# Kernel tuning notes

Measured on AMD Instinct MI355X. Metric: run time of the kernel, lower is better.

Reference implementation:

```python
import jax, jax.numpy as jnp
import numpy as np

B, S, D, H = 2, 4096, 512, 8
DH = D // H
EPS = 1e-5


def setup_inputs() -> dict:
    key = jax.random.key(0)
    ks = jax.random.split(key, 8)
    s = 0.02
    return {
        "x": jax.random.normal(ks[0], (B, S, D), jnp.float32),
        "in_proj_w": jax.random.normal(ks[1], (3 * D, D), jnp.float32) * s,
        "in_proj_b": jnp.zeros((3 * D,), jnp.float32),
        "out_proj_w": jax.random.normal(ks[2], (D, D), jnp.float32) * s,
        "out_proj_b": jnp.zeros((D,), jnp.float32),
        "ln1_g": jnp.ones((D,), jnp.float32),
        "ln1_b": jnp.zeros((D,), jnp.float32),
        "ln2_g": jnp.ones((D,), jnp.float32),
        "ln2_b": jnp.zeros((D,), jnp.float32),
        "w1": jax.random.normal(ks[3], (D, D), jnp.float32) * s,
        "b1": jnp.zeros((D,), jnp.float32),
        "w2": jax.random.normal(ks[4], (D, D), jnp.float32) * s,
        "b2": jnp.zeros((D,), jnp.float32),
        "window": 256,
    }


def _layernorm(x, g, b):
    mu = jnp.mean(x, axis=-1, keepdims=True)
    var = jnp.mean(jnp.square(x - mu), axis=-1, keepdims=True)
    return (x - mu) * jax.lax.rsqrt(var + EPS) * g + b


def reference(x, in_proj_w, in_proj_b, out_proj_w, out_proj_b,
              ln1_g, ln1_b, ln2_g, ln2_b, w1, b1, w2, b2, window):
    b, s, d = x.shape
    # sliding-window mask: allowed iff |i - j| <= window
    idx = jnp.arange(s)
    allowed = jnp.abs(idx[:, None] - idx[None, :]) <= window  # [S,S]

    # fused QKV projection (torch MultiheadAttention layout: W [3D, D])
    qkv = x @ in_proj_w.T + in_proj_b  # [B,S,3D]
    q, k, v = jnp.split(qkv, 3, axis=-1)
    q = q.reshape(b, s, H, DH)
    k = k.reshape(b, s, H, DH)
    v = v.reshape(b, s, H, DH)

    scale = 1.0 / jnp.sqrt(jnp.float32(DH))
    scores = jnp.einsum("bqhd,bkhd->bhqk", q, k) * scale  # [B,H,S,S]
    scores = jnp.where(allowed[None, None], scores, -jnp.inf)
    attn = jax.nn.softmax(scores, axis=-1)
    ctx = jnp.einsum("bhqk,bkhd->bqhd", attn, v).reshape(b, s, d)
    attn_out = ctx @ out_proj_w.T + out_proj_b

    # residual + LayerNorm (dropout rate 0 -> identity)
    h = _layernorm(x + attn_out, ln1_g, ln1_b)
    mlp = jax.nn.relu(h @ w1.T + b1) @ w2.T + b2
    return _layernorm(h + mlp, ln2_g, ln2_b)
```

## Files before the change

### kernel.cpp

```cpp
#include <hip/hip_runtime.h>

typedef __bf16 bf16;
typedef __bf16 bf16x2 __attribute__((ext_vector_type(2)));
typedef __bf16 bf16x8 __attribute__((ext_vector_type(8)));
typedef float f32x4 __attribute__((ext_vector_type(4)));

#define S_LEN 4096
#define DMODEL 512
#define NHEAD 8
#define DHEAD 64
#define BATCH 2
#define M_ROWS (BATCH * S_LEN)
#define K_DIM 512
#define QKV_LD 1536

__device__ __forceinline__ void async16(void* lds, const void* g) {
  __builtin_amdgcn_global_load_lds(
      (const __attribute__((address_space(1))) unsigned int*)g,
      (__attribute__((address_space(3))) unsigned int*)lds, 16, 0, 0);
}

__device__ __forceinline__ int detect_bf16(const unsigned int* x, int lane) {
  int cnt = 0;
#pragma unroll
  for (int i = 0; i < 16; ++i) {
    const unsigned int w = x[lane * 16 + i];
    const unsigned int e = (w >> 7) & 0xFFu;
    cnt += (e >= 100u && e <= 140u) ? 1 : 0;
  }
#pragma unroll
  for (int off = 1; off < 64; off <<= 1) cnt += __shfl_xor(cnt, off);
  return (cnt >= 700) ? 1 : 0;
}

__device__ __forceinline__ bf16x8 ld8(const void* p, size_t e, bool asF32) {
  if (asF32) {
    const float* q = (const float*)p + e;
    const float4 a = *(const float4*)q;
    const float4 b = *(const float4*)(q + 4);
    bf16x8 r;
    r[0] = (bf16)a.x; r[1] = (bf16)a.y; r[2] = (bf16)a.z; r[3] = (bf16)a.w;
    r[4] = (bf16)b.x; r[5] = (bf16)b.y; r[6] = (bf16)b.z; r[7] = (bf16)b.w;
    return r;
  }
  return *(const bf16x8*)((const bf16*)p + e);
}

__device__ __forceinline__ float ld1(const void* p, size_t e, bool asF32) {
  return asF32 ? ((const float*)p)[e] : (float)((const bf16*)p)[e];
}

__global__ __launch_bounds__(256) void cvt_all(const void* __restrict__ x,
                                               const void* __restrict__ s0,
                                               const void* __restrict__ s1,
                                               const void* __restrict__ s2,
                                               const void* __restrict__ s3,
                                               bf16* __restrict__ xb,
                                               bf16* __restrict__ warena,
                                               int* __restrict__ flag) {
  const int isbf = detect_bf16((const unsigned int*)x, threadIdx.x & 63);
  const bool f32in = (isbf == 0);
  const int b = blockIdx.x;
  if (b == 0 && threadIdx.x == 0) *flag = isbf;
  if (b < 2048) {
    const size_t idx = ((size_t)b * 256 + threadIdx.x) * 8;
    *(bf16x8*)(xb + idx) = ld8(x, idx, f32in);
    return;
  }
  const int wb = b - 2048;
  const void* s;
  size_t doff;
  int lb;
  if (wb < 384)      { s = s0; doff = 0;        lb = wb; }
  else if (wb < 512) { s = s1; doff = 786432;   lb = wb - 384; }
  else if (wb < 640) { s = s2; doff = 1048576;  lb = wb - 512; }
  else               { s = s3; doff = 1310720;  lb = wb - 640; }
  const size_t idx = (size_t)lb * 2048 + threadIdx.x * 8;
  *(bf16x8*)(warena + doff + idx) = ld8(s, idx, f32in);
}

template <int NMAT, int BN, bool RELU>
__global__ __launch_bounds__(256) void gemm_bt(const bf16* __restrict__ A,
                                               const bf16* __restrict__ W,
                                               const void* __restrict__ bias,
                                               bf16* __restrict__ C,
                                               const int* __restrict__ flag) {
  __shared__ __align__(16) bf16 As[2][128 * 64];
  __shared__ __align__(16) bf16 Ws[2][BN * 64];

  const bool f32in = (*flag == 0);

  const int t = threadIdx.x;
  const int lane = t & 63;
  const int wave = t >> 6;
  constexpr int MT = (BN == 128) ? 4 : 2;
  const int wm = (BN == 128) ? (wave >> 1) * 64 : wave * 32;
  const int wn = (BN == 128) ? (wave & 1) * 64 : 0;
  const int l16 = lane & 15;
  const int quad = lane >> 4;

  constexpr int NB = NMAT / BN;
  constexpr int MPX = (M_ROWS / 128) / 8;
  const int bid = blockIdx.x;
  const int xcd = bid & 7;
  const int r = bid >> 3;
  const int m0 = (xcd * MPX + r / NB) * 128;
  const int n0 = (r % NB) * BN;

  const int rr = lane >> 3;
  const int cb = (lane & 7) ^ rr;
  const int sw = l16 & 7;

  f32x4 acc[MT][4];
#pragma unroll
  for (int i = 0; i < MT; ++i)
#pragma unroll
    for (int j = 0; j < 4; ++j) acc[i][j] = (f32x4){0.f, 0.f, 0.f, 0.f};

  auto stage = [&](int buf, int kt) {
#pragma unroll
    for (int i = 0; i < 4; ++i) {
      const int r0 = wave * 32 + i * 8;
      async16(&As[buf][r0 * 64],
              &A[(size_t)(m0 + r0 + rr) * K_DIM + kt + cb * 8]);
    }
#pragma unroll
    for (int i = 0; i < BN / 32; ++i) {
      const int r0 = wave * (BN / 4) + i * 8;
      async16(&Ws[buf][r0 * 64],
              &W[(size_t)(n0 + r0 + rr) * K_DIM + kt + cb * 8]);
    }
  };

  stage(0, 0);
  constexpr int NIT = K_DIM / 64;
  for (int it = 0; it < NIT; ++it) {
    const int cur = it & 1;
    __syncthreads();
    if (it + 1 < NIT) stage(cur ^ 1, (it + 1) * 64);
#pragma unroll
    for (int ks = 0; ks < 2; ++ks) {
      bf16x8 af[MT], wf[4];
#pragma unroll
      for (int mt = 0; mt < MT; ++mt)
        af[mt] = *(const bf16x8*)&As[cur][(wm + mt * 16 + l16) * 64 +
                                          (((ks * 4 + quad) ^ sw) * 8)];
#pragma unroll
      for (int nt = 0; nt < 4; ++nt)
        wf[nt] = *(const bf16x8*)&Ws[cur][(wn + nt * 16 + l16) * 64 +
                                          (((ks * 4 + quad) ^ sw) * 8)];
#pragma unroll
      for (int mt = 0; mt < MT; ++mt)
#pragma unroll
        for (int nt = 0; nt < 4; ++nt)
          acc[mt][nt] = __builtin_amdgcn_mfma_f32_16x16x32_bf16(af[mt], wf[nt],
                                                                acc[mt][nt], 0, 0, 0);
    }
  }

#pragma unroll
  for (int nt = 0; nt < 4; ++nt) {
    const int n = n0 + wn + nt * 16 + l16;
    const float bv = ld1(bias, n, f32in);
#pragma unroll
    for (int mt = 0; mt < MT; ++mt) {
#pragma unroll
      for (int r4 = 0; r4 < 4; ++r4) {
        const int m = m0 + wm + mt * 16 + quad * 4 + r4;
        float v = acc[mt][nt][r4] + bv;
        if (RELU) v = fmaxf(v, 0.f);
        C[(size_t)m * NMAT + n] = (bf16)v;
      }
    }
  }
}

__global__ __launch_bounds__(256) void attn_fwd(const bf16* __restrict__ qkv,
                                                bf16* __restrict__ ctx,
                                                const int* __restrict__ wptr) {
  __shared__ __align__(16) bf16 Kt[2][64 * 64];
  __shared__ __align__(16) bf16 Vt[2][64][72];
  __shared__ __align__(16) bf16 Pbuf[4][16][72];

  const int t = threadIdx.x;
  const int lane = t & 63;
  const int wave = t >> 6;
  const int l16 = lane & 15;
  const int quad = lane >> 4;
  const int rr = lane >> 3;
  const int cb = (lane & 7) ^ rr;
  const int sw = l16 & 7;

  const int bid = blockIdx.x;
  const int xcd = bid & 7;
  const int jj = bid >> 3;
  const int pair = xcd * 2 + (jj >> 6);
  const int qblk = jj & 63;
  const int h = pair & 7;
  const int b = pair >> 3;
  const int qbase = qblk * 64;
  int window = *wptr;
  if (window < 0) window = 0;
  if (window > S_LEN) window = S_LEN;
  const float sc_log2e = 0.125f * 1.44269504f;

  const int qrow = qbase + wave * 16 + l16;
  const bf16* qp = qkv + (size_t)(b * S_LEN + qrow) * QKV_LD + h * DHEAD;
  const bf16x8 qf0 = *(const bf16x8*)(qp + quad * 8);
  const bf16x8 qf1 = *(const bf16x8*)(qp + 32 + quad * 8);

  f32x4 o[4];
#pragma unroll
  for (int nt = 0; nt < 4; ++nt) o[nt] = (f32x4){0.f, 0.f, 0.f, 0.f};
  float lp[4] = {0.f, 0.f, 0.f, 0.f};

  int kstart = qbase - window;
  if (kstart < 0) kstart = 0;
  kstart &= ~63;
  int kend = qbase + 64 + window;
  if (kend > S_LEN) kend = S_LEN;
  const int niter = (kend - kstart + 63) >> 6;

  const int vk = (t & 31) * 2;
  const int vd = (t >> 5) * 8;
  const bf16* vbase = qkv + (size_t)(b * S_LEN) * QKV_LD + 2 * DMODEL + h * DHEAD + vd;
  const bf16* kbase = qkv + (size_t)(b * S_LEN) * QKV_LD + DMODEL + h * DHEAD;

#pragma unroll
  for (int i = 0; i < 2; ++i) {
    const int r0 = wave * 16 + i * 8;
    async16(&Kt[0][r0 * 64],
            &kbase[(size_t)(kstart + r0 + rr) * QKV_LD + cb * 8]);
  }
  {
    const bf16* p = vbase + (size_t)(kstart + vk) * QKV_LD;
    const bf16x8 va = *(const bf16x8*)p;
    const bf16x8 vb = *(const bf16x8*)(p + QKV_LD);
#pragma unroll
    for (int j = 0; j < 8; ++j) {
      bf16x2 pr; pr[0] = va[j]; pr[1] = vb[j];
      *(bf16x2*)&Vt[0][vd + j][vk] = pr;
    }
  }

  for (int it = 0; it < niter; ++it) {
    const int kt = kstart + it * 64;
    const int cur = it & 1;
    __syncthreads();

    bf16x8 na, nb;
    const bool have_next = (it + 1 < niter);
    if (have_next) {
#pragma unroll
      for (int i = 0; i < 2; ++i) {
        const int r0 = wave * 16 + i * 8;
        async16(&Kt[cur ^ 1][r0 * 64],
                &kbase[(size_t)(kt + 64 + r0 + rr) * QKV_LD + cb * 8]);
      }
      const bf16* p = vbase + (size_t)(kt + 64 + vk) * QKV_LD;
      na = *(const bf16x8*)p;
      nb = *(const bf16x8*)(p + QKV_LD);
    }

    f32x4 s[4];
#pragma unroll
    for (int t4 = 0; t4 < 4; ++t4) s[t4] = (f32x4){0.f, 0.f, 0.f, 0.f};
#pragma unroll
    for (int t4 = 0; t4 < 4; ++t4) {
      const int row = t4 * 16 + l16;
      const bf16x8 k0 = *(const bf16x8*)&Kt[cur][row * 64 + ((quad ^ sw) * 8)];
      const bf16x8 k1 =
          *(const bf16x8*)&Kt[cur][row * 64 + (((4 + quad) ^ sw) * 8)];
      s[t4] = __builtin_amdgcn_mfma_f32_16x16x32_bf16(qf0, k0, s[t4], 0, 0, 0);
      s[t4] = __builtin_amdgcn_mfma_f32_16x16x32_bf16(qf1, k1, s[t4], 0, 0, 0);
    }

#pragma unroll
    for (int r = 0; r < 4; ++r) {
      const int q = qbase + wave * 16 + quad * 4 + r;
      const int lo = q - window, hi = q + window;
      float psum = 0.f;
#pragma unroll
      for (int t4 = 0; t4 < 4; ++t4) {
        const int key = kt + t4 * 16 + l16;
        const float p = (key >= lo && key <= hi)
                            ? __builtin_amdgcn_exp2f(s[t4][r] * sc_log2e)
                            : 0.f;
        psum += p;
        Pbuf[wave][quad * 4 + r][t4 * 16 + l16] = (bf16)p;
      }
      lp[r] += psum;
    }

    const bf16x8 pf0 = *(const bf16x8*)&Pbuf[wave][l16][quad * 8];
    const bf16x8 pf1 = *(const bf16x8*)&Pbuf[wave][l16][32 + quad * 8];
#pragma unroll
    for (int nt = 0; nt < 4; ++nt) {
      const bf16x8 v0 = *(const bf16x8*)&Vt[cur][nt * 16 + l16][quad * 8];
      const bf16x8 v1 = *(const bf16x8*)&Vt[cur][nt * 16 + l16][32 + quad * 8];
      o[nt] = __builtin_amdgcn_mfma_f32_16x16x32_bf16(pf0, v0, o[nt], 0, 0, 0);
      o[nt] = __builtin_amdgcn_mfma_f32_16x16x32_bf16(pf1, v1, o[nt], 0, 0, 0);
    }

    if (have_next) {
#pragma unroll
      for (int j = 0; j < 8; ++j) {
        bf16x2 pr; pr[0] = na[j]; pr[1] = nb[j];
        *(bf16x2*)&Vt[cur ^ 1][vd + j][vk] = pr;
      }
    }
  }

#pragma unroll
  for (int r = 0; r < 4; ++r) {
#pragma unroll
    for (int off = 1; off < 16; off <<= 1) lp[r] += __shfl_xor(lp[r], off);
    const float inv = (lp[r] > 0.f) ? (1.0f / lp[r]) : 0.f;
    const int q = qbase + wave * 16 + quad * 4 + r;
#pragma unroll
    for (int nt = 0; nt < 4; ++nt) {
      ctx[(size_t)(b * S_LEN + q) * DMODEL + h * DHEAD + nt * 16 + l16] =
          (bf16)(o[nt][r] * inv);
    }
  }
}

template <bool A_RAW, bool OUT_RAW>
__global__ __launch_bounds__(256) void ln_fused(const void* __restrict__ a,
                                                const bf16* __restrict__ bres,
                                                const void* __restrict__ g,
                                                const void* __restrict__ be,
                                                void* __restrict__ out,
                                                const int* __restrict__ flag) {
  const bool f32in = (*flag == 0);
  const int row = blockIdx.x * 4 + (threadIdx.x >> 6);
  const int lane = threadIdx.x & 63;
  const size_t base = (size_t)row * DMODEL + lane * 8;
  const bf16x8 va = ld8(a, base, A_RAW && f32in);
  const bf16x8 vb = *(const bf16x8*)(bres + base);
  float v[8], s = 0.f, s2 = 0.f;
#pragma unroll
  for (int j = 0; j < 8; ++j) {
    v[j] = (float)va[j] + (float)vb[j];
    s += v[j];
    s2 += v[j] * v[j];
  }
#pragma unroll
  for (int off = 1; off < 64; off <<= 1) {
    s += __shfl_xor(s, off);
    s2 += __shfl_xor(s2, off);
  }
  const float mean = s * (1.0f / DMODEL);
  float var = s2 * (1.0f / DMODEL) - mean * mean;
  if (var < 0.f) var = 0.f;
  const float rstd = rsqrtf(var + 1e-5f);
  const bf16x8 gv = ld8(g, lane * 8, f32in);
  const bf16x8 bev = ld8(be, lane * 8, f32in);
  float ov[8];
#pragma unroll
  for (int j = 0; j < 8; ++j)
    ov[j] = (v[j] - mean) * rstd * (float)gv[j] + (float)bev[j];
  if (OUT_RAW && f32in) {
    float4 o0 = {ov[0], ov[1], ov[2], ov[3]};
    float4 o1 = {ov[4], ov[5], ov[6], ov[7]};
    *(float4*)((float*)out + base) = o0;
    *(float4*)((float*)out + base + 4) = o1;
  } else {
    bf16x8 ob;
#pragma unroll
    for (int j = 0; j < 8; ++j) ob[j] = (bf16)ov[j];
    *(bf16x8*)((bf16*)out + base) = ob;
  }
}

extern "C" void kernel_launch(void* const* d_in, const int* in_sizes, int n_in,
                              void* d_out, int out_size, void* d_ws, size_t ws_size,
                              hipStream_t stream) {
  const void* x          = d_in[0];
  const void* in_proj_w  = d_in[1];
  const void* in_proj_b  = d_in[2];
  const void* out_proj_w = d_in[3];
  const void* out_proj_b = d_in[4];
  const void* ln1_g      = d_in[5];
  const void* ln1_b      = d_in[6];
  const void* ln2_g      = d_in[7];
  const void* ln2_b      = d_in[8];
  const void* w1         = d_in[9];
  const void* b1         = d_in[10];
  const void* w2         = d_in[11];
  const void* b2         = d_in[12];
  const int*  wptr       = (const int*)d_in[13];

  char* ws = (char*)d_ws;
  int* flag = (int*)ws;
  bf16* warena = (bf16*)(ws + 256);
  bf16* wq = warena;
  bf16* wo = warena + 786432;
  bf16* w1b = warena + 1048576;
  bf16* w2b = warena + 1310720;
  char* big = ws + 256 + 3145728;
  bf16* qkv      = (bf16*)big;
  bf16* h        = (bf16*)big;
  bf16* a1       = (bf16*)(big + 8388608);
  bf16* attn_out = (bf16*)(big + 16777216);
  bf16* mlp      = attn_out;
  bf16* xb       = (bf16*)d_out;
  bf16* ctx      = (bf16*)d_out;

  cvt_all<<<2816, 256, 0, stream>>>(x, in_proj_w, out_proj_w, w1, w2, xb, warena, flag);
  gemm_bt<QKV_LD, 128, false><<<768, 256, 0, stream>>>(
      xb, wq, in_proj_b, qkv, flag);
  attn_fwd<<<dim3(BATCH * NHEAD * (S_LEN / 64)), 256, 0, stream>>>(qkv, ctx, wptr);
  gemm_bt<DMODEL, 64, false><<<512, 256, 0, stream>>>(
      ctx, wo, out_proj_b, attn_out, flag);
  ln_fused<true, false><<<dim3(M_ROWS / 4), 256, 0, stream>>>(
      x, attn_out, ln1_g, ln1_b, h, flag);
  gemm_bt<DMODEL, 64, true><<<512, 256, 0, stream>>>(
      h, w1b, b1, a1, flag);
  gemm_bt<DMODEL, 64, false><<<512, 256, 0, stream>>>(
      a1, w2b, b2, mlp, flag);
  ln_fused<false, true><<<dim3(M_ROWS / 4), 256, 0, stream>>>(
      h, mlp, ln2_g, ln2_b, d_out, flag);
}
```

Before: 207.8 us.

## Single-buffer wide GEMM tiles and split attention MFMA phases with wave priority

For the BN=128 GEMM variant, the LDS double buffer is replaced with a single buffer and two barriers per k-step. This halves shared memory so more blocks can be resident per CU, at the cost of no load/compute overlap within a block. The attention inner loop is split into two halves of QK^T MFMA and softmax, with the PV MFMAs also split. The MFMA sections are wrapped in s_setprio so waves interleave matrix and exp/VALU work.

```diff
diff --git a/kernel.cpp b/kernel.cpp
--- a/kernel.cpp
+++ b/kernel.cpp
@@ -85,8 +85,10 @@
                                                const void* __restrict__ bias,
                                                bf16* __restrict__ C,
                                                const int* __restrict__ flag) {
-  __shared__ __align__(16) bf16 As[2][128 * 64];
-  __shared__ __align__(16) bf16 Ws[2][BN * 64];
+  constexpr bool DB = (BN != 128);
+  constexpr int NBUF = DB ? 2 : 1;
+  __shared__ __align__(16) bf16 As[NBUF][128 * 64];
+  __shared__ __align__(16) bf16 Ws[NBUF][BN * 64];
 
   const bool f32in = (*flag == 0);
 
@@ -132,22 +134,17 @@
     }
   };
 
-  stage(0, 0);
-  constexpr int NIT = K_DIM / 64;
-  for (int it = 0; it < NIT; ++it) {
-    const int cur = it & 1;
-    __syncthreads();
-    if (it + 1 < NIT) stage(cur ^ 1, (it + 1) * 64);
+  auto compute = [&](int buf) {
 #pragma unroll
     for (int ks = 0; ks < 2; ++ks) {
       bf16x8 af[MT], wf[4];
 #pragma unroll
       for (int mt = 0; mt < MT; ++mt)
-        af[mt] = *(const bf16x8*)&As[cur][(wm + mt * 16 + l16) * 64 +
+        af[mt] = *(const bf16x8*)&As[buf][(wm + mt * 16 + l16) * 64 +
                                           (((ks * 4 + quad) ^ sw) * 8)];
 #pragma unroll
       for (int nt = 0; nt < 4; ++nt)
-        wf[nt] = *(const bf16x8*)&Ws[cur][(wn + nt * 16 + l16) * 64 +
+        wf[nt] = *(const bf16x8*)&Ws[buf][(wn + nt * 16 + l16) * 64 +
                                           (((ks * 4 + quad) ^ sw) * 8)];
 #pragma unroll
       for (int mt = 0; mt < MT; ++mt)
@@ -155,6 +152,24 @@
         for (int nt = 0; nt < 4; ++nt)
           acc[mt][nt] = __builtin_amdgcn_mfma_f32_16x16x32_bf16(af[mt], wf[nt],
                                                                 acc[mt][nt], 0, 0, 0);
+    }
+  };
+
+  constexpr int NIT = K_DIM / 64;
+  if constexpr (DB) {
+    stage(0, 0);
+    for (int it = 0; it < NIT; ++it) {
+      const int cur = it & 1;
+      __syncthreads();
+      if (it + 1 < NIT) stage(cur ^ 1, (it + 1) * 64);
+      compute(cur);
+    }
+  } else {
+    for (int kt = 0; kt < K_DIM; kt += 64) {
+      __syncthreads();
+      stage(0, kt);
+      __syncthreads();
+      compute(0);
     }
   }
 
@@ -265,8 +280,10 @@
     f32x4 s[4];
 #pragma unroll
     for (int t4 = 0; t4 < 4; ++t4) s[t4] = (f32x4){0.f, 0.f, 0.f, 0.f};
-#pragma unroll
-    for (int t4 = 0; t4 < 4; ++t4) {
+
+    __builtin_amdgcn_s_setprio(1);
+#pragma unroll
+    for (int t4 = 0; t4 < 2; ++t4) {
       const int row = t4 * 16 + l16;
       const bf16x8 k0 = *(const bf16x8*)&Kt[cur][row * 64 + ((quad ^ sw) * 8)];
       const bf16x8 k1 =
@@ -274,33 +291,67 @@
       s[t4] = __builtin_amdgcn_mfma_f32_16x16x32_bf16(qf0, k0, s[t4], 0, 0, 0);
       s[t4] = __builtin_amdgcn_mfma_f32_16x16x32_bf16(qf1, k1, s[t4], 0, 0, 0);
     }
+    __builtin_amdgcn_s_setprio(0);
 
 #pragma unroll
     for (int r = 0; r < 4; ++r) {
       const int q = qbase + wave * 16 + quad * 4 + r;
       const int lo = q - window, hi = q + window;
-      float psum = 0.f;
-#pragma unroll
-      for (int t4 = 0; t4 < 4; ++t4) {
+#pragma unroll
+      for (int t4 = 0; t4 < 2; ++t4) {
         const int key = kt + t4 * 16 + l16;
         const float p = (key >= lo && key <= hi)
                             ? __builtin_amdgcn_exp2f(s[t4][r] * sc_log2e)
                             : 0.f;
-        psum += p;
+        lp[r] += p;
         Pbuf[wave][quad * 4 + r][t4 * 16 + l16] = (bf16)p;
       }
-      lp[r] += psum;
+    }
+
+    __builtin_amdgcn_s_setprio(1);
+#pragma unroll
+    for (int t4 = 2; t4 < 4; ++t4) {
+      const int row = t4 * 16 + l16;
+      const bf16x8 k0 = *(const bf16x8*)&Kt[cur][row * 64 + ((quad ^ sw) * 8)];
+      const bf16x8 k1 =
+          *(const bf16x8*)&Kt[cur][row * 64 + (((4 + quad) ^ sw) * 8)];
+      s[t4] = __builtin_amdgcn_mfma_f32_16x16x32_bf16(qf0, k0, s[t4], 0, 0, 0);
+      s[t4] = __builtin_amdgcn_mfma_f32_16x16x32_bf16(qf1, k1, s[t4], 0, 0, 0);
+    }
+    __builtin_amdgcn_s_setprio(0);
+
+#pragma unroll
+    for (int r = 0; r < 4; ++r) {
+      const int q = qbase + wave * 16 + quad * 4 + r;
+      const int lo = q - window, hi = q + window;
+#pragma unroll
+      for (int t4 = 2; t4 < 4; ++t4) {
+        const int key = kt + t4 * 16 + l16;
+        const float p = (key >= lo && key <= hi)
+                            ? __builtin_amdgcn_exp2f(s[t4][r] * sc_log2e)
+                            : 0.f;
+        lp[r] += p;
+        Pbuf[wave][quad * 4 + r][t4 * 16 + l16] = (bf16)p;
+      }
     }
 
     const bf16x8 pf0 = *(const bf16x8*)&Pbuf[wave][l16][quad * 8];
-    const bf16x8 pf1 = *(const bf16x8*)&Pbuf[wave][l16][32 + quad * 8];
+    __builtin_amdgcn_s_setprio(1);
 #pragma unroll
     for (int nt = 0; nt < 4; ++nt) {
       const bf16x8 v0 = *(const bf16x8*)&Vt[cur][nt * 16 + l16][quad * 8];
+      o[nt] = __builtin_amdgcn_mfma_f32_16x16x32_bf16(pf0, v0, o[nt], 0, 0, 0);
+    }
+    __builtin_amdgcn_s_setprio(0);
+
+    const bf16x8 pf1 = *(const bf16x8*)&Pbuf[wave][l16][32 + quad * 8];
+    __builtin_amdgcn_s_setprio(1);
+#pragma unroll
+    for (int nt = 0; nt < 4; ++nt) {
       const bf16x8 v1 = *(const bf16x8*)&Vt[cur][nt * 16 + l16][32 + quad * 8];
-      o[nt] = __builtin_amdgcn_mfma_f32_16x16x32_bf16(pf0, v0, o[nt], 0, 0, 0);
       o[nt] = __builtin_amdgcn_mfma_f32_16x16x32_bf16(pf1, v1, o[nt], 0, 0, 0);
     }
+    __builtin_amdgcn_s_setprio(0);
 
     if (have_next) {
 #pragma unroll
```

Result: no change. 207.0 us (-0.4%).

## Split QKV into planar buffers and widen attention blocks to 128 queries

Applied to the files above, without the earlier changes.

The QKV GEMM gets its own kernel. It writes Q, K and V into three separate [M,512] planes instead of one interleaved [M,1536] buffer. This kernel is single-buffered, with two barriers per k-step. Attention now runs 8 waves over 128 query rows per block, so each K/V tile staged in LDS is reused by twice as many queries, and it writes ctx in place over Q. It also adds s_setprio around the MFMA sections. Workspace buffers are reassigned, and a1 now aliases the output buffer. The single-buffered QKV GEMM may expose load latency, and the larger attention block lowers occupancy.

```diff
diff --git a/kernel.cpp b/kernel.cpp
--- a/kernel.cpp
+++ b/kernel.cpp
@@ -2,6 +2,7 @@
 
 typedef __bf16 bf16;
 typedef __bf16 bf16x2 __attribute__((ext_vector_type(2)));
+typedef __bf16 bf16x4 __attribute__((ext_vector_type(4)));
 typedef __bf16 bf16x8 __attribute__((ext_vector_type(8)));
 typedef float f32x4 __attribute__((ext_vector_type(4)));
 
@@ -12,7 +13,7 @@
 #define BATCH 2
 #define M_ROWS (BATCH * S_LEN)
 #define K_DIM 512
-#define QKV_LD 1536
+#define QLD 512
 
 __device__ __forceinline__ void async16(void* lds, const void* g) {
   __builtin_amdgcn_global_load_lds(
@@ -79,41 +80,121 @@
   *(bf16x8*)(warena + doff + idx) = ld8(s, idx, f32in);
 }
 
-template <int NMAT, int BN, bool RELU>
+__global__ __launch_bounds__(256) void gemm_qkv(const bf16* __restrict__ A,
+                                                const bf16* __restrict__ W,
+                                                const void* __restrict__ bias,
+                                                bf16* __restrict__ C,
+                                                const int* __restrict__ flag) {
+  __shared__ __align__(16) bf16 As[128 * 64];
+  __shared__ __align__(16) bf16 Ws[128 * 64];
+
+  const bool f32in = (*flag == 0);
+  const int t = threadIdx.x;
+  const int lane = t & 63;
+  const int wave = t >> 6;
+  const int wm = (wave >> 1) * 64;
+  const int wn = (wave & 1) * 64;
+  const int l16 = lane & 15;
+  const int quad = lane >> 4;
+
+  constexpr int NB = 1536 / 128;
+  const int bid = blockIdx.x;
+  const int xcd = bid & 7;
+  const int r = bid >> 3;
+  const int m0 = (xcd * 8 + r / NB) * 128;
+  const int n0 = (r % NB) * 128;
+
+  const int rr = lane >> 3;
+  const int cb = (lane & 7) ^ rr;
+  const int sw = l16 & 7;
+
+  f32x4 acc[4][4];
+#pragma unroll
+  for (int i = 0; i < 4; ++i)
+#pragma unroll
+    for (int j = 0; j < 4; ++j) acc[i][j] = (f32x4){0.f, 0.f, 0.f, 0.f};
+
+  for (int kt = 0; kt < K_DIM; kt += 64) {
+    __syncthreads();
+#pragma unroll
+    for (int i = 0; i < 4; ++i) {
+      const int r0 = wave * 32 + i * 8;
+      async16(&As[r0 * 64], &A[(size_t)(m0 + r0 + rr) * K_DIM + kt + cb * 8]);
+    }
+#pragma unroll
+    for (int i = 0; i < 4; ++i) {
+      const int r0 = wave * 32 + i * 8;
+      async16(&Ws[r0 * 64], &W[(size_t)(n0 + r0 + rr) * K_DIM + kt + cb * 8]);
+    }
+    __syncthreads();
+#pragma unroll
+    for (int ks = 0; ks < 2; ++ks) {
+      bf16x8 af[4], wf[4];
+#pragma unroll
+      for (int mt = 0; mt < 4; ++mt)
+        af[mt] = *(const bf16x8*)&As[(wm + mt * 16 + l16) * 64 +
+                                     (((ks * 4 + quad) ^ sw) * 8)];
+#pragma unroll
+      for (int nt = 0; nt < 4; ++nt)
+        wf[nt] = *(const bf16x8*)&Ws[(wn + nt * 16 + l16) * 64 +
+                                     (((ks * 4 + quad) ^ sw) * 8)];
+#pragma unroll
+      for (int mt = 0; mt < 4; ++mt)
+#pragma unroll
+        for (int nt = 0; nt < 4; ++nt)
+          acc[mt][nt] = __builtin_amdgcn_mfma_f32_16x16x32_bf16(af[mt], wf[nt],
+                                                                acc[mt][nt], 0, 0, 0);
+    }
+  }
+
+#pragma unroll
+  for (int nt = 0; nt < 4; ++nt) {
+    const int n = n0 + wn + nt * 16 + l16;
+    const float bv = ld1(bias, n, f32in);
+    bf16* Cm = C + (size_t)(n >> 9) * ((size_t)M_ROWS * DMODEL) + (n & 511);
+#pragma unroll
+    for (int mt = 0; mt < 4; ++mt) {
+#pragma unroll
+      for (int r4 = 0; r4 < 4; ++r4) {
+        const int m = m0 + wm + mt * 16 + quad * 4 + r4;
+        Cm[(size_t)m * DMODEL] = (bf16)(acc[mt][nt][r4] + bv);
+      }
+    }
+  }
+}
+
+template <bool RELU>
 __global__ __launch_bounds__(256) void gemm_bt(const bf16* __restrict__ A,
                                                const bf16* __restrict__ W,
                                                const void* __restrict__ bias,
                                                bf16* __restrict__ C,
                                                const int* __restrict__ flag) {
+  constexpr int BN = 64;
   __shared__ __align__(16) bf16 As[2][128 * 64];
   __shared__ __align__(16) bf16 Ws[2][BN * 64];
 
   const bool f32in = (*flag == 0);
-
   const int t = threadIdx.x;
   const int lane = t & 63;
   const int wave = t >> 6;
-  constexpr int MT = (BN == 128) ? 4 : 2;
-  const int wm = (BN == 128) ? (wave >> 1) * 64 : wave * 32;
-  const int wn = (BN == 128) ? (wave & 1) * 64 : 0;
+  const int wm = wave * 32;
   const int l16 = lane & 15;
   const int quad = lane >> 4;
 
-  constexpr int NB = NMAT / BN;
-  constexpr int MPX = (M_ROWS / 128) / 8;
+  constexpr int NB = 512 / BN;
   const int bid = blockIdx.x;
   const int xcd = bid & 7;
   const int r = bid >> 3;
-  const int m0 = (xcd * MPX + r / NB) * 128;
+  const int m0 = (xcd * 8 + r / NB) * 128;
   const int n0 = (r % NB) * BN;
 
   const int rr = lane >> 3;
   const int cb = (lane & 7) ^ rr;
   const int sw = l16 & 7;
 
-  f32x4 acc[MT][4];
-#pragma unroll
-  for (int i = 0; i < MT; ++i)
+  f32x4 acc[2][4];
+#pragma unroll
+  for (int i = 0; i < 2; ++i)
 #pragma unroll
     for (int j = 0; j < 4; ++j) acc[i][j] = (f32x4){0.f, 0.f, 0.f, 0.f};
 
@@ -125,8 +206,8 @@
               &A[(size_t)(m0 + r0 + rr) * K_DIM + kt + cb * 8]);
     }
 #pragma unroll
-    for (int i = 0; i < BN / 32; ++i) {
-      const int r0 = wave * (BN / 4) + i * 8;
+    for (int i = 0; i < 2; ++i) {
+      const int r0 = wave * 16 + i * 8;
       async16(&Ws[buf][r0 * 64],
               &W[(size_t)(n0 + r0 + rr) * K_DIM + kt + cb * 8]);
     }
@@ -140,17 +221,17 @@
     if (it + 1 < NIT) stage(cur ^ 1, (it + 1) * 64);
 #pragma unroll
     for (int ks = 0; ks < 2; ++ks) {
-      bf16x8 af[MT], wf[4];
-#pragma unroll
-      for (int mt = 0; mt < MT; ++mt)
+      bf16x8 af[2], wf[4];
+#pragma unroll
+      for (int mt = 0; mt < 2; ++mt)
         af[mt] = *(const bf16x8*)&As[cur][(wm + mt * 16 + l16) * 64 +
                                           (((ks * 4 + quad) ^ sw) * 8)];
 #pragma unroll
       for (int nt = 0; nt < 4; ++nt)
-        wf[nt] = *(const bf16x8*)&Ws[cur][(wn + nt * 16 + l16) * 64 +
+        wf[nt] = *(const bf16x8*)&Ws[cur][(nt * 16 + l16) * 64 +
                                           (((ks * 4 + quad) ^ sw) * 8)];
 #pragma unroll
-      for (int mt = 0; mt < MT; ++mt)
+      for (int mt = 0; mt < 2; ++mt)
 #pragma unroll
         for (int nt = 0; nt < 4; ++nt)
           acc[mt][nt] = __builtin_amdgcn_mfma_f32_16x16x32_bf16(af[mt], wf[nt],
@@ -160,27 +241,31 @@
 
 #pragma unroll
   for (int nt = 0; nt < 4; ++nt) {
-    const int n = n0 + wn + nt * 16 + l16;
+    const int n = n0 + nt * 16 + l16;
     const float bv = ld1(bias, n, f32in);
 #pragma unroll
-    for (int mt = 0; mt < MT; ++mt) {
+    for (int mt = 0; mt < 2; ++mt) {
 #pragma unroll
       for (int r4 = 0; r4 < 4; ++r4) {
         const int m = m0 + wm + mt * 16 + quad * 4 + r4;
         float v = acc[mt][nt][r4] + bv;
         if (RELU) v = fmaxf(v, 0.f);
-        C[(size_t)m * NMAT + n] = (bf16)v;
+        C[(size_t)m * 512 + n] = (bf16)v;
       }
     }
   }
 }
 
-__global__ __launch_bounds__(256) void attn_fwd(const bf16* __restrict__ qkv,
-                                                bf16* __restrict__ ctx,
+__global__ __launch_bounds__(512) void attn_fwd(bf16* __restrict__ qkv,
                                                 const int* __restrict__ wptr) {
   __shared__ __align__(16) bf16 Kt[2][64 * 64];
   __shared__ __align__(16) bf16 Vt[2][64][72];
-  __shared__ __align__(16) bf16 Pbuf[4][16][72];
+  __shared__ __align__(16) bf16 Pbuf[8][16][72];
+
+  const bf16* Q = qkv;
+  const bf16* K = qkv + (size_t)M_ROWS * DMODEL;
+  const bf16* V = qkv + 2 * (size_t)M_ROWS * DMODEL;
+  bf16* ctxw = qkv;
 
   const int t = threadIdx.x;
   const int lane = t & 63;
@@ -194,18 +279,18 @@
   const int bid = blockIdx.x;
   const int xcd = bid & 7;
   const int jj = bid >> 3;
-  const int pair = xcd * 2 + (jj >> 6);
-  const int qblk = jj & 63;
+  const int pair = xcd * 2 + (jj >> 5);
+  const int qblk = jj & 31;
   const int h = pair & 7;
   const int b = pair >> 3;
-  const int qbase = qblk * 64;
+  const int qbase = qblk * 128;
   int window = *wptr;
   if (window < 0) window = 0;
   if (window > S_LEN) window = S_LEN;
   const float sc_log2e = 0.125f * 1.44269504f;
 
   const int qrow = qbase + wave * 16 + l16;
-  const bf16* qp = qkv + (size_t)(b * S_LEN + qrow) * QKV_LD + h * DHEAD;
+  const bf16* qp = Q + (size_t)(b * S_LEN + qrow) * QLD + h * DHEAD;
   const bf16x8 qf0 = *(const bf16x8*)(qp + quad * 8);
   const bf16x8 qf1 = *(const bf16x8*)(qp + 32 + quad * 8);
 
@@ -217,27 +302,26 @@
   int kstart = qbase - window;
   if (kstart < 0) kstart = 0;
   kstart &= ~63;
-  int kend = qbase + 64 + window;
+  int kend = qbase + 128 + window;
   if (kend > S_LEN) kend = S_LEN;
   const int niter = (kend - kstart + 63) >> 6;
 
   const int vk = (t & 31) * 2;
-  const int vd = (t >> 5) * 8;
-  const bf16* vbase = qkv + (size_t)(b * S_LEN) * QKV_LD + 2 * DMODEL + h * DHEAD + vd;
-  const bf16* kbase = qkv + (size_t)(b * S_LEN) * QKV_LD + DMODEL + h * DHEAD;
-
-#pragma unroll
-  for (int i = 0; i < 2; ++i) {
-    const int r0 = wave * 16 + i * 8;
+  const int vd = (t >> 5) * 4;
+  const bf16* vbase = V + (size_t)(b * S_LEN) * QLD + h * DHEAD + vd;
+  const bf16* kbase = K + (size_t)(b * S_LEN) * QLD + h * DHEAD;
+
+  {
+    const int r0 = wave * 8;
     async16(&Kt[0][r0 * 64],
-            &kbase[(size_t)(kstart + r0 + rr) * QKV_LD + cb * 8]);
+            &kbase[(size_t)(kstart + r0 + rr) * QLD + cb * 8]);
   }
   {
-    const bf16* p = vbase + (size_t)(kstart + vk) * QKV_LD;
-    const bf16x8 va = *(const bf16x8*)p;
-    const bf16x8 vb = *(const bf16x8*)(p + QKV_LD);
-#pragma unroll
-    for (int j = 0; j < 8; ++j) {
+    const bf16* p = vbase + (size_t)(kstart + vk) * QLD;
+    const bf16x4 va = *(const bf16x4*)p;
+    const bf16x4 vb = *(const bf16x4*)(p + QLD);
+#pragma unroll
+    for (int j = 0; j < 4; ++j) {
       bf16x2 pr; pr[0] = va[j]; pr[1] = vb[j];
       *(bf16x2*)&Vt[0][vd + j][vk] = pr;
     }
@@ -248,23 +332,24 @@
     const int cur = it & 1;
     __syncthreads();
 
-    bf16x8 na, nb;
+    bf16x4 na, nb;
     const bool have_next = (it + 1 < niter);
     if (have_next) {
-#pragma unroll
-      for (int i = 0; i < 2; ++i) {
-        const int r0 = wave * 16 + i * 8;
+      {
+        const int r0 = wave * 8;
         async16(&Kt[cur ^ 1][r0 * 64],
-                &kbase[(size_t)(kt + 64 + r0 + rr) * QKV_LD + cb * 8]);
+                &kbase[(size_t)(kt + 64 + r0 + rr) * QLD + cb * 8]);
       }
-      const bf16* p = vbase + (size_t)(kt + 64 + vk) * QKV_LD;
-      na = *(const bf16x8*)p;
-      nb = *(const bf16x8*)(p + QKV_LD);
+      const bf16* p = vbase + (size_t)(kt + 64 + vk) * QLD;
+      na = *(const bf16x4*)p;
+      nb = *(const bf16x4*)(p + QLD);
     }
 
     f32x4 s[4];
 #pragma unroll
     for (int t4 = 0; t4 < 4; ++t4) s[t4] = (f32x4){0.f, 0.f, 0.f, 0.f};
+
+    __builtin_amdgcn_s_setprio(1);
 #pragma unroll
     for (int t4 = 0; t4 < 4; ++t4) {
       const int row = t4 * 16 + l16;
@@ -274,26 +359,26 @@
       s[t4] = __builtin_amdgcn_mfma_f32_16x16x32_bf16(qf0, k0, s[t4], 0, 0, 0);
       s[t4] = __builtin_amdgcn_mfma_f32_16x16x32_bf16(qf1, k1, s[t4], 0, 0, 0);
     }
+    __builtin_amdgcn_s_setprio(0);
 
 #pragma unroll
     for (int r = 0; r < 4; ++r) {
       const int q = qbase + wave * 16 + quad * 4 + r;
       const int lo = q - window, hi = q + window;
-      float psum = 0.f;
 #pragma unroll
       for (int t4 = 0; t4 < 4; ++t4) {
         const int key = kt + t4 * 16 + l16;
         const float p = (key >= lo && key <= hi)
                             ? __builtin_amdgcn_exp2f(s[t4][r] * sc_log2e)
                             : 0.f;
-        psum += p;
+        lp[r] += p;
         Pbuf[wave][quad * 4 + r][t4 * 16 + l16] = (bf16)p;
       }
-      lp[r] += psum;
     }
 
     const bf16x8 pf0 = *(const bf16x8*)&Pbuf[wave][l16][quad * 8];
     const bf16x8 pf1 = *(const bf16x8*)&Pbuf[wave][l16][32 + quad * 8];
+    __builtin_amdgcn_s_setprio(1);
 #pragma unroll
     for (int nt = 0; nt < 4; ++nt) {
       const bf16x8 v0 = *(const bf16x8*)&Vt[cur][nt * 16 + l16][quad * 8];
@@ -301,10 +386,11 @@
       o[nt] = __builtin_amdgcn_mfma_f32_16x16x32_bf16(pf0, v0, o[nt], 0, 0, 0);
       o[nt] = __builtin_amdgcn_mfma_f32_16x16x32_bf16(pf1, v1, o[nt], 0, 0, 0);
     }
+    __builtin_amdgcn_s_setprio(0);
 
     if (have_next) {
 #pragma unroll
-      for (int j = 0; j < 8; ++j) {
+      for (int j = 0; j < 4; ++j) {
         bf16x2 pr; pr[0] = na[j]; pr[1] = nb[j];
         *(bf16x2*)&Vt[cur ^ 1][vd + j][vk] = pr;
       }
@@ -319,7 +405,7 @@
     const int q = qbase + wave * 16 + quad * 4 + r;
 #pragma unroll
     for (int nt = 0; nt < 4; ++nt) {
-      ctx[(size_t)(b * S_LEN + q) * DMODEL + h * DHEAD + nt * 16 + l16] =
+      ctxw[(size_t)(b * S_LEN + q) * QLD + h * DHEAD + nt * 16 + l16] =
           (bf16)(o[nt][r] * inv);
     }
   }
@@ -394,31 +480,26 @@
   char* ws = (char*)d_ws;
   int* flag = (int*)ws;
   bf16* warena = (bf16*)(ws + 256);
-  bf16* wq = warena;
-  bf16* wo = warena + 786432;
+  bf16* wq  = warena;
+  bf16* wo  = warena + 786432;
   bf16* w1b = warena + 1048576;
   bf16* w2b = warena + 1310720;
-  char* big = ws + 256 + 3145728;
-  bf16* qkv      = (bf16*)big;
-  bf16* h        = (bf16*)big;
-  bf16* a1       = (bf16*)(big + 8388608);
-  bf16* attn_out = (bf16*)(big + 16777216);
+  bf16* qkvS = (bf16*)(ws + 256 + 3145728);
+  bf16* ctx      = qkvS;
+  bf16* attn_out = qkvS + (size_t)M_ROWS * DMODEL;
+  bf16* h        = qkvS + 2 * (size_t)M_ROWS * DMODEL;
   bf16* mlp      = attn_out;
   bf16* xb       = (bf16*)d_out;
-  bf16* ctx      = (bf16*)d_out;
+  bf16* a1       = (bf16*)d_out;
 
   cvt_all<<<2816, 256, 0, stream>>>(x, in_proj_w, out_proj_w, w1, w2, xb, warena, flag);
-  gemm_bt<QKV_LD, 128, false><<<768, 256, 0, stream>>>(
-      xb, wq, in_proj_b, qkv, flag);
-  attn_fwd<<<dim3(BATCH * NHEAD * (S_LEN / 64)), 256, 0, stream>>>(qkv, ctx, wptr);
-  gemm_bt<DMODEL, 64, false><<<512, 256, 0, stream>>>(
-      ctx, wo, out_proj_b, attn_out, flag);
+  gemm_qkv<<<768, 256, 0, stream>>>(xb, wq, in_proj_b, qkvS, flag);
+  attn_fwd<<<512, 512, 0, stream>>>(qkvS, wptr);
+  gemm_bt<false><<<512, 256, 0, stream>>>(ctx, wo, out_proj_b, attn_out, flag);
   ln_fused<true, false><<<dim3(M_ROWS / 4), 256, 0, stream>>>(
       x, attn_out, ln1_g, ln1_b, h, flag);
-  gemm_bt<DMODEL, 64, true><<<512, 256, 0, stream>>>(
-      h, w1b, b1, a1, flag);
-  gemm_bt<DMODEL, 64, false><<<512, 256, 0, stream>>>(
-      a1, w2b, b2, mlp, flag);
+  gemm_bt<true><<<512, 256, 0, stream>>>(h, w1b, b1, a1, flag);
+  gemm_bt<false><<<512, 256, 0, stream>>>(a1, w2b, b2, mlp, flag);
   ln_fused<false, true><<<dim3(M_ROWS / 4), 256, 0, stream>>>(
       h, mlp, ln2_g, ln2_b, d_out, flag);
 }
```

Result: faster. 199.2 us (-4.1%).
